# Performance work log

Hardware: AMD Instinct MI355X
Metric: run time of the kernel (lower is better)

Reference implementation:

```python
import jax, jax.numpy as jnp
import numpy as np

# Assumed sub-module definitions (NODETracker repo, sources not provided):
#   MLP(in,out)   = Linear -> LayerNorm -> LeakyReLU(0.1)
#   MLPODEF(dim,hidden,n_layers=2) = Linear(dim->h) -> tanh -> [Linear(h->h) -> tanh]*(n_layers-1) -> Linear(h->dim)
#   ode_solver_factory(None) -> fixed-step RK4, here 4 steps over t in [0,1]

LEAKY = 0.1
N_ODE_STEPS = 4
LATENT_DIM = 512
OBS_DIM = 256
HID_DIM = 1024
STATE = 2 * LATENT_DIM  # 1024
TIME_LEN = 128
BATCH = 512


def mlp_block(x, W, b, g, beta):
    h = x @ W + b
    mu = h.mean(-1, keepdims=True)
    var = ((h - mu) ** 2).mean(-1, keepdims=True)
    h = (h - mu) * jax.lax.rsqrt(var + 1e-5) * g + beta
    return jnp.where(h >= 0, h, LEAKY * h)


def odef(z, p):
    W0, b0, W1, b1, W2, b2 = p
    h = jnp.tanh(z @ W0 + b0)
    h = jnp.tanh(h @ W1 + b1)
    return h @ W2 + b2


def rk4_solve(z, p):
    dt = 1.0 / N_ODE_STEPS
    def step(z, _):
        k1 = odef(z, p)
        k2 = odef(z + 0.5 * dt * k1, p)
        k3 = odef(z + 0.5 * dt * k2, p)
        k4 = odef(z + dt * k3, p)
        return z + (dt / 6.0) * (k1 + 2 * k2 + 2 * k3 + k4), None
    z, _ = jax.lax.scan(step, z, None, length=N_ODE_STEPS)
    return z


def gru_step(x, h, W_ih, W_hh, b_ih, b_hh):
    gi = x @ W_ih.T + b_ih
    gh = h @ W_hh.T + b_hh
    i_r, i_z, i_n = jnp.split(gi, 3, axis=-1)
    h_r, h_z, h_n = jnp.split(gh, 3, axis=-1)
    r = jax.nn.sigmoid(i_r + h_r)
    zg = jax.nn.sigmoid(i_z + h_z)
    n = jnp.tanh(i_n + r * h_n)
    return (1.0 - zg) * n + zg * h


def setup_inputs() -> dict:
    key = jax.random.key(0)
    ks = jax.random.split(key, 16)
    def lin(k, fi, fo):
        return jax.random.normal(k, (fi, fo), jnp.float32) / np.sqrt(fi)
    return {
        'xs': jax.random.normal(ks[0], (TIME_LEN, BATCH, OBS_DIM), jnp.float32),
        'obs_W': lin(ks[1], OBS_DIM, HID_DIM), 'obs_b': jnp.zeros((HID_DIM,), jnp.float32),
        'obs_g': jnp.ones((HID_DIM,), jnp.float32), 'obs_beta': jnp.zeros((HID_DIM,), jnp.float32),
        'lat_W': lin(ks[2], HID_DIM, STATE), 'lat_b': jnp.zeros((STATE,), jnp.float32),
        'lat_g': jnp.ones((STATE,), jnp.float32), 'lat_beta': jnp.zeros((STATE,), jnp.float32),
        'ode_W0': lin(ks[3], STATE, HID_DIM), 'ode_b0': jnp.zeros((HID_DIM,), jnp.float32),
        'ode_W1': lin(ks[4], HID_DIM, HID_DIM), 'ode_b1': jnp.zeros((HID_DIM,), jnp.float32),
        'ode_W2': lin(ks[5], HID_DIM, STATE), 'ode_b2': jnp.zeros((STATE,), jnp.float32),
        'gru_Wih': jax.random.normal(ks[6], (3 * STATE, STATE), jnp.float32) / np.sqrt(STATE),
        'gru_Whh': jax.random.normal(ks[7], (3 * STATE, STATE), jnp.float32) / np.sqrt(STATE),
        'gru_bih': jnp.zeros((3 * STATE,), jnp.float32),
        'gru_bhh': jnp.zeros((3 * STATE,), jnp.float32),
    }


def reference(xs, obs_W, obs_b, obs_g, obs_beta, lat_W, lat_b, lat_g, lat_beta,
              ode_W0, ode_b0, ode_W1, ode_b1, ode_W2, ode_b2,
              gru_Wih, gru_Whh, gru_bih, gru_bhh):
    hs = mlp_block(xs, obs_W, obs_b, obs_g, obs_beta)          # [T,B,hid]
    zs = mlp_block(hs, lat_W, lat_b, lat_g, lat_beta)          # [T,B,2*latent]
    ode_p = (ode_W0, ode_b0, ode_W1, ode_b1, ode_W2, ode_b2)
    batch = xs.shape[1]
    h0 = jnp.zeros((batch, STATE), xs.dtype)

    def step(h, z_t):
        z = rk4_solve(z_t, ode_p)                               # NODE solve from t=0 to 1
        h_new = gru_step(z, h, gru_Wih, gru_Whh, gru_bih, gru_bhh)
        return h_new, None

    z0, _ = jax.lax.scan(step, h0, zs)                          # [B,2*latent]
    return z0[:, :LATENT_DIM], z0[:, LATENT_DIM:]
```

## Files before the change

### kernel.cpp

```cpp
#include <hip/hip_runtime.h>
#include <hip/hip_bf16.h>
#include <hip/hip_cooperative_groups.h>

namespace cg = cooperative_groups;

typedef __bf16 bf16_t;
typedef __bf16 bf16x8 __attribute__((ext_vector_type(8)));
typedef float f32x4 __attribute__((ext_vector_type(4)));

#define TLEN 128
#define BATCHN 512
#define OBS 256
#define HID 1024
#define STATEDIM 1024
#define ROWS (TLEN * BATCHN)
#define RKDT 0.25f

enum { EPI_F32 = 0, EPI_GI, EPI_TANH, EPI_Z0, EPI_KG, EPI_K1, EPI_K2, EPI_K3, EPI_K4 };

__device__ __forceinline__ void gload_lds16(const bf16_t* g, bf16_t* l) {
  __builtin_amdgcn_global_load_lds(
      (const __attribute__((address_space(1))) void*)g,
      (__attribute__((address_space(3))) void*)l, 16, 0, 0);
}

__device__ __forceinline__ bf16_t f2bf(float x) { return (bf16_t)x; }

__device__ __forceinline__ float fast_tanh(float x) {
  const float e = __expf(2.f * x);
  return 1.f - 2.f / (e + 1.f);
}
__device__ __forceinline__ float fast_sigmoid(float x) {
  return 1.f / (1.f + __expf(-x));
}

#define MF(a_, b_, c_) __builtin_amdgcn_mfma_f32_16x16x32_bf16(a_, b_, c_, 0, 0, 0)

template<int EPI>
__global__ __launch_bounds__(256)
void gemm_bt(const bf16_t* __restrict__ A, const bf16_t* __restrict__ Wt,
             const float* __restrict__ bias, int M, int N, int K,
             float* __restrict__ outF, bf16_t* __restrict__ outB,
             float* __restrict__ Z, float* __restrict__ ZN,
             bf16_t* __restrict__ S2, const float* __restrict__ Z0,
             float kgc)
{
  __shared__ __align__(16) bf16_t As[2][128 * 32];
  __shared__ __align__(16) bf16_t Bs[2][128 * 32];
  const int tid = threadIdx.x;
  const int lane = tid & 63;
  const int wave = tid >> 6;
  const int nbn = N >> 7;

  int bid = blockIdx.x;
  {
    const int nwg = gridDim.x;
    const int q = nwg >> 3, r = nwg & 7;
    const int xcd = bid & 7, lid = bid >> 3;
    bid = (xcd < r ? xcd * (q + 1) : r * (q + 1) + (xcd - r) * q) + lid;
  }
  const int bm = bid / nbn;
  const int bn = bid % nbn;
  const int m0 = bm << 7, n0 = bn << 7;
  const int wr = wave >> 1, wc = wave & 1;
  const int srow = tid >> 2;
  const int scol = (tid & 3) << 3;

  f32x4 acc[4][4] = {};
  const int nk = K >> 5;
  int cur = 0;

  {
    const bf16_t* ga = A  + (size_t)(m0 + srow) * K + scol;
    const bf16_t* gb = Wt + (size_t)(n0 + srow) * K + scol;
    bf16_t* la = &As[0][tid * 8];
    bf16_t* lb = &Bs[0][tid * 8];
    gload_lds16(ga, la);
    gload_lds16(ga + (size_t)64 * K, la + 2048);
    gload_lds16(gb, lb);
    gload_lds16(gb + (size_t)64 * K, lb + 2048);
  }

  for (int ks = 0; ks < nk; ++ks) {
    __syncthreads();
    if (ks + 1 < nk) {
      const bf16_t* ga = A  + (size_t)(m0 + srow) * K + (ks + 1) * 32 + scol;
      const bf16_t* gb = Wt + (size_t)(n0 + srow) * K + (ks + 1) * 32 + scol;
      bf16_t* la = &As[cur ^ 1][tid * 8];
      bf16_t* lb = &Bs[cur ^ 1][tid * 8];
      gload_lds16(ga, la);
      gload_lds16(ga + (size_t)64 * K, la + 2048);
      gload_lds16(gb, lb);
      gload_lds16(gb + (size_t)64 * K, lb + 2048);
    }
    const int kb = (lane >> 4) << 3;
    const int rr = lane & 15;
    bf16x8 af[4], bfr[4];
#pragma unroll
    for (int i = 0; i < 4; ++i) {
      af[i]  = *(const bf16x8*)&As[cur][(wr * 64 + i * 16 + rr) * 32 + kb];
      bfr[i] = *(const bf16x8*)&Bs[cur][(wc * 64 + i * 16 + rr) * 32 + kb];
    }
#pragma unroll
    for (int i = 0; i < 4; ++i)
#pragma unroll
      for (int j = 0; j < 4; ++j)
        acc[i][j] = MF(af[i], bfr[j], acc[i][j]);
    cur ^= 1;
  }

  const int cb = n0 + wc * 64 + (lane & 15);
  const int rb = m0 + wr * 64 + ((lane >> 4) << 2);
#pragma unroll
  for (int j = 0; j < 4; ++j) {
    const int c = cb + j * 16;
    float bv = 0.f;
    if constexpr (EPI != EPI_F32 && EPI != EPI_KG) bv = bias[c];
#pragma unroll
    for (int i = 0; i < 4; ++i) {
      const int r0 = rb + i * 16;
#pragma unroll
      for (int r = 0; r < 4; ++r) {
        const size_t idx = (size_t)(r0 + r) * N + c;
        const float v = acc[i][j][r];
        if constexpr (EPI == EPI_F32) {
          outF[idx] = v;
        } else if constexpr (EPI == EPI_GI) {
          outF[idx] = v + bv;
        } else if constexpr (EPI == EPI_TANH) {
          outB[idx] = f2bf(fast_tanh(v + bv));
        } else if constexpr (EPI == EPI_Z0) {
          const float t = v + bv;
          outF[idx] = t;
          outB[idx] = f2bf(fast_tanh(t));
        } else if constexpr (EPI == EPI_KG) {
          outB[idx] = f2bf(fast_tanh(Z0[idx] + kgc * v));
        } else if constexpr (EPI == EPI_K1) {
          const float k = v + bv;
          ZN[idx] = Z[idx] + (RKDT / 6.f) * k;
          outB[idx] = f2bf(k);
        } else if constexpr (EPI == EPI_K2 || EPI == EPI_K3) {
          const float k = v + bv;
          ZN[idx] += (RKDT / 3.f) * k;
          outB[idx] = f2bf(k);
        } else {
          const float k = v + bv;
          const float s = ZN[idx] + (RKDT / 6.f) * k;
          Z[idx] = s;
          const size_t si = (size_t)(r0 + r) * 2048 + c;
          const bf16_t hi = f2bf(s);
          S2[si] = hi;
          S2[si + 1024] = f2bf(s - (float)hi);
        }
      }
    }
  }
}

__global__ __launch_bounds__(512)
void gru_persistent(const float* __restrict__ gi,
                    const bf16_t* __restrict__ Whh,
                    const float* __restrict__ bhh,
                    float* __restrict__ Hf,
                    bf16_t* __restrict__ hb,
                    float* __restrict__ outp,
                    int TS, int t0)
{
  __shared__ __align__(16) bf16_t Bs[48 * 1032];
  const int tid  = threadIdx.x;
  const int lane = tid & 63;
  const int w    = tid >> 6;
  const int rg   = blockIdx.x >> 6;
  const int jg   = blockIdx.x & 63;
  const int r0   = rg << 7;
  const int j0   = jg << 4;

  for (int it = tid; it < 48 * 128; it += 512) {
    const int rr = it >> 7;
    const int co = (it & 127) << 3;
    const int g = rr >> 4, c = rr & 15;
    *(bf16x8*)&Bs[rr * 1032 + co] =
        *(const bf16x8*)&Whh[(size_t)(g * 1024 + j0 + c) * 1024 + co];
  }

  const int myj = j0 + (lane & 15);
  const float bh_r = bhh[myj], bh_z = bhh[1024 + myj], bh_n = bhh[2048 + myj];
  const int rbase = r0 + w * 16 + ((lane >> 4) << 2);

  float h[4];
#pragma unroll
  for (int q = 0; q < 4; ++q) h[q] = Hf[(size_t)(rbase + q) * 1024 + myj];

  __syncthreads();
  cg::grid_group grid = cg::this_grid();

  const int arow = r0 + w * 16 + (lane & 15);
  const int akoff = (lane >> 4) << 3;

  for (int t = t0; t < t0 + TS; ++t) {
    const bf16_t* ap = hb + (size_t)(t & 1) * 512 * 2048 +
                       (size_t)arow * 2048 + akoff;
    f32x4 a0 = {}, a1 = {}, a2 = {};
    const bf16_t* bp0 = &Bs[(0  + (lane & 15)) * 1032 + akoff];
    const bf16_t* bp1 = &Bs[(16 + (lane & 15)) * 1032 + akoff];
    const bf16_t* bp2 = &Bs[(32 + (lane & 15)) * 1032 + akoff];
#pragma unroll 8
    for (int kc = 0; kc < 64; ++kc) {
      const bf16x8 af = *(const bf16x8*)(ap + kc * 32);
      const int kl = (kc * 32) & 1023;
      a0 = MF(af, *(const bf16x8*)(bp0 + kl), a0);
      a1 = MF(af, *(const bf16x8*)(bp1 + kl), a1);
      a2 = MF(af, *(const bf16x8*)(bp2 + kl), a2);
    }
    const float* gir = gi + (size_t)(t - t0) * 512 * 3072;
    bf16_t* hbw = hb + (size_t)((t + 1) & 1) * 512 * 2048;
#pragma unroll
    for (int q = 0; q < 4; ++q) {
      const size_t rr = (size_t)(rbase + q);
      const float ir = gir[rr * 3072 + myj];
      const float iz = gir[rr * 3072 + 1024 + myj];
      const float in = gir[rr * 3072 + 2048 + myj];
      const float rg_ = fast_sigmoid(ir + a0[q] + bh_r);
      const float zg  = fast_sigmoid(iz + a1[q] + bh_z);
      const float n   = fast_tanh(in + rg_ * (a2[q] + bh_n));
      h[q] = (1.f - zg) * n + zg * h[q];
      const bf16_t hi = f2bf(h[q]);
      hbw[rr * 2048 + myj] = hi;
      hbw[rr * 2048 + 1024 + myj] = f2bf(h[q] - (float)hi);
    }
    grid.sync();
  }

#pragma unroll
  for (int q = 0; q < 4; ++q) {
    const int r = rbase + q;
    Hf[(size_t)r * 1024 + myj] = h[q];
    if (myj < 512) outp[(size_t)r * 512 + myj] = h[q];
    else           outp[262144 + (size_t)r * 512 + (myj - 512)] = h[q];
  }
}

template<bool SPLIT>
__global__ __launch_bounds__(256)
void ln_leaky(const float* __restrict__ pre, const float* __restrict__ b,
              const float* __restrict__ g, const float* __restrict__ bet,
              bf16_t* __restrict__ outB, float* __restrict__ zf)
{
  const int row = blockIdx.x;
  const int tid = threadIdx.x;
  const float* p = pre + (size_t)row * 1024;
  float v[4];
  float s = 0.f, s2 = 0.f;
#pragma unroll
  for (int i = 0; i < 4; ++i) {
    const int c = tid + i * 256;
    v[i] = p[c] + b[c];
    s += v[i]; s2 += v[i] * v[i];
  }
#pragma unroll
  for (int o = 32; o; o >>= 1) { s += __shfl_down(s, o); s2 += __shfl_down(s2, o); }
  __shared__ float rs[4], rs2[4];
  if ((tid & 63) == 0) { rs[tid >> 6] = s; rs2[tid >> 6] = s2; }
  __syncthreads();
  s = rs[0] + rs[1] + rs[2] + rs[3];
  s2 = rs2[0] + rs2[1] + rs2[2] + rs2[3];
  const float mu = s * (1.f / 1024.f);
  const float var = s2 * (1.f / 1024.f) - mu * mu;
  const float rstd = rsqrtf(var + 1e-5f);
#pragma unroll
  for (int i = 0; i < 4; ++i) {
    const int c = tid + i * 256;
    float h = (v[i] - mu) * rstd * g[c] + bet[c];
    h = h >= 0.f ? h : 0.1f * h;
    if constexpr (SPLIT) {
      const bf16_t hi = f2bf(h);
      outB[(size_t)row * 2048 + c] = hi;
      outB[(size_t)row * 2048 + 1024 + c] = f2bf(h - (float)hi);
      zf[(size_t)row * 1024 + c] = h;
    } else {
      outB[(size_t)row * 1024 + c] = f2bf(h);
    }
  }
}

__global__ __launch_bounds__(256)
void transpose_bf16(const float* __restrict__ in, bf16_t* __restrict__ out, int R, int C)
{
  __shared__ float t[32][33];
  const int c0 = blockIdx.x * 32, r0 = blockIdx.y * 32;
  const int tx = threadIdx.x & 31, ty = threadIdx.x >> 5;
#pragma unroll
  for (int i = 0; i < 32; i += 8)
    t[ty + i][tx] = in[(size_t)(r0 + ty + i) * C + c0 + tx];
  __syncthreads();
#pragma unroll
  for (int i = 0; i < 32; i += 8)
    out[(size_t)(c0 + ty + i) * R + r0 + tx] = f2bf(t[tx][ty + i]);
}

__global__ __launch_bounds__(256)
void f2b_kernel(const float* __restrict__ in, bf16_t* __restrict__ out, int n)
{
  const int i = blockIdx.x * 256 + threadIdx.x;
  if (i < n) out[i] = f2bf(in[i]);
}

__global__ __launch_bounds__(256)
void dup2_kernel(const bf16_t* __restrict__ in, bf16_t* __restrict__ out, int N, int K)
{
  const int idx = blockIdx.x * 256 + threadIdx.x;
  if (idx >= N * 2 * K) return;
  const int n = idx / (2 * K);
  const int kk = idx - n * 2 * K;
  const int k = kk < K ? kk : kk - K;
  out[idx] = in[(size_t)n * K + k];
}

__global__ void sentinel_kernel(float* out, float code) {
  if (threadIdx.x == 0 && blockIdx.x == 0) out[0] = code;
}

extern "C" void kernel_launch(void* const* d_in, const int* in_sizes, int n_in,
                              void* d_out, int out_size, void* d_ws, size_t ws_size,
                              hipStream_t stream)
{
  const float* xs    = (const float*)d_in[0];
  const float* obs_W = (const float*)d_in[1];
  const float* obs_b = (const float*)d_in[2];
  const float* obs_g = (const float*)d_in[3];
  const float* obs_be= (const float*)d_in[4];
  const float* lat_W = (const float*)d_in[5];
  const float* lat_b = (const float*)d_in[6];
  const float* lat_g = (const float*)d_in[7];
  const float* lat_be= (const float*)d_in[8];
  const float* W0    = (const float*)d_in[9];
  const float* b0    = (const float*)d_in[10];
  const float* W1    = (const float*)d_in[11];
  const float* b1    = (const float*)d_in[12];
  const float* W2    = (const float*)d_in[13];
  const float* b2    = (const float*)d_in[14];
  const float* Wih   = (const float*)d_in[15];
  const float* Whh   = (const float*)d_in[16];
  const float* bih   = (const float*)d_in[17];
  const float* bhh   = (const float*)d_in[18];

  char* ws = (char*)d_ws;
  size_t off = 0;
  auto alloc = [&](size_t bytes) { char* p = ws + off; off += bytes; return p; };

  bf16_t* OBSWT = (bf16_t*)alloc((size_t)HID * OBS * 2);
  bf16_t* LATWT = (bf16_t*)alloc((size_t)STATEDIM * HID * 2);
  bf16_t* W0T   = (bf16_t*)alloc((size_t)HID * STATEDIM * 2);
  bf16_t* W0T2  = (bf16_t*)alloc((size_t)HID * 2048 * 2);
  bf16_t* W1T   = (bf16_t*)alloc((size_t)HID * HID * 2);
  bf16_t* W2T   = (bf16_t*)alloc((size_t)STATEDIM * HID * 2);
  bf16_t* WIH2  = (bf16_t*)alloc((size_t)3072 * 2048 * 2);
  bf16_t* WHHB  = (bf16_t*)alloc((size_t)3072 * 1024 * 2);
  float*  Hf    = (float*)alloc((size_t)512 * 1024 * 4);
  bf16_t* HB2   = (bf16_t*)alloc((size_t)2 * 512 * 2048 * 2);
  bf16_t* WIHB  = (bf16_t*)alloc((size_t)3072 * 1024 * 2);
  bf16_t* XSB   = (bf16_t*)alloc((size_t)ROWS * OBS * 2);
  const size_t staticEnd = off;

  int nc = -1;
  const int ncs[8] = {1, 2, 4, 8, 16, 32, 64, 128};
  for (int i = 0; i < 8; ++i) {
    const size_t R = (size_t)ROWS / ncs[i];
    if (staticEnd + R * 22528 <= ws_size) { nc = ncs[i]; break; }
  }
  if (nc < 0) {
    sentinel_kernel<<<1, 1, 0, stream>>>((float*)d_out,
                                         -(1000000.0f + (float)(ws_size >> 20)));
    return;
  }
  const int R = ROWS / nc;
  char* arena = ws + staticEnd;
  float*  A1f  = (float*)(arena);
  float*  A2f  = (float*)(arena + (size_t)R * 4096);
  float*  Z0f  = (float*)(arena + (size_t)R * 8192);
  bf16_t* H1b  = (bf16_t*)(arena + (size_t)R * 12288);
  bf16_t* H2b  = (bf16_t*)(arena + (size_t)R * 14336);
  bf16_t* KB   = (bf16_t*)(arena + (size_t)R * 16384);
  bf16_t* S2b  = (bf16_t*)(arena + (size_t)R * 18432);
  float*  GIf  = (float*)(arena);

  auto gemm = [&](int epi, const bf16_t* A, const bf16_t* Wt, const float* bias,
                  int M, int N, int K, float* oF, bf16_t* oB, float kgc = 0.f) {
    dim3 g((M / 128) * (N / 128)), b(256);
    switch (epi) {
      case EPI_F32:  gemm_bt<EPI_F32><<<g, b, 0, stream>>>(A, Wt, bias, M, N, K, oF, oB, A2f, A1f, S2b, Z0f, kgc); break;
      case EPI_GI:   gemm_bt<EPI_GI><<<g, b, 0, stream>>>(A, Wt, bias, M, N, K, oF, oB, A2f, A1f, S2b, Z0f, kgc); break;
      case EPI_TANH: gemm_bt<EPI_TANH><<<g, b, 0, stream>>>(A, Wt, bias, M, N, K, oF, oB, A2f, A1f, S2b, Z0f, kgc); break;
      case EPI_Z0:   gemm_bt<EPI_Z0><<<g, b, 0, stream>>>(A, Wt, bias, M, N, K, oF, oB, A2f, A1f, S2b, Z0f, kgc); break;
      case EPI_KG:   gemm_bt<EPI_KG><<<g, b, 0, stream>>>(A, Wt, bias, M, N, K, oF, oB, A2f, A1f, S2b, Z0f, kgc); break;
      case EPI_K1:   gemm_bt<EPI_K1><<<g, b, 0, stream>>>(A, Wt, bias, M, N, K, oF, oB, A2f, A1f, S2b, Z0f, kgc); break;
      case EPI_K2:   gemm_bt<EPI_K2><<<g, b, 0, stream>>>(A, Wt, bias, M, N, K, oF, oB, A2f, A1f, S2b, Z0f, kgc); break;
      case EPI_K3:   gemm_bt<EPI_K3><<<g, b, 0, stream>>>(A, Wt, bias, M, N, K, oF, oB, A2f, A1f, S2b, Z0f, kgc); break;
      case EPI_K4:   gemm_bt<EPI_K4><<<g, b, 0, stream>>>(A, Wt, bias, M, N, K, oF, oB, A2f, A1f, S2b, Z0f, kgc); break;
    }
  };

  transpose_bf16<<<dim3(HID / 32, OBS / 32), 256, 0, stream>>>(obs_W, OBSWT, OBS, HID);
  transpose_bf16<<<dim3(STATEDIM / 32, HID / 32), 256, 0, stream>>>(lat_W, LATWT, HID, STATEDIM);
  transpose_bf16<<<dim3(HID / 32, STATEDIM / 32), 256, 0, stream>>>(W0, W0T, STATEDIM, HID);
  dup2_kernel<<<(HID * 2048) / 256, 256, 0, stream>>>(W0T, W0T2, HID, 1024);
  transpose_bf16<<<dim3(HID / 32, HID / 32), 256, 0, stream>>>(W1, W1T, HID, HID);
  transpose_bf16<<<dim3(STATEDIM / 32, HID / 32), 256, 0, stream>>>(W2, W2T, HID, STATEDIM);
  f2b_kernel<<<(3072 * 1024) / 256, 256, 0, stream>>>(Wih, WIHB, 3072 * 1024);
  dup2_kernel<<<(3072 * 2048) / 256, 256, 0, stream>>>(WIHB, WIH2, 3072, 1024);
  f2b_kernel<<<(3072 * 1024) / 256, 256, 0, stream>>>(Whh, WHHB, 3072 * 1024);
  f2b_kernel<<<(ROWS * OBS) / 256, 256, 0, stream>>>(xs, XSB, ROWS * OBS);

  hipMemsetAsync(Hf, 0, (size_t)512 * 1024 * 4, stream);
  hipMemsetAsync(HB2, 0, (size_t)2 * 512 * 2048 * 2, stream);
  const int TS = R / BATCHN;

  for (int c = 0; c < nc; ++c) {
    gemm(EPI_F32, XSB + (size_t)c * R * OBS, OBSWT, nullptr, R, HID, OBS, A1f, nullptr);
    ln_leaky<false><<<R, 256, 0, stream>>>(A1f, obs_b, obs_g, obs_be, H1b, nullptr);
    gemm(EPI_F32, H1b, LATWT, nullptr, R, STATEDIM, HID, A1f, nullptr);
    ln_leaky<true><<<R, 256, 0, stream>>>(A1f, lat_b, lat_g, lat_be, S2b, A2f);

    for (int step = 0; step < 4; ++step) {
      gemm(EPI_Z0, S2b, W0T2, b0, R, HID, 2048, Z0f, H1b);
      gemm(EPI_TANH, H1b, W1T, b1, R, HID, HID, nullptr, H2b);
      gemm(EPI_K1, H2b, W2T, b2, R, STATEDIM, HID, nullptr, KB);
      for (int stg = 1; stg < 4; ++stg) {
        const float cg = (stg < 3) ? 0.5f * RKDT : RKDT;
        gemm(EPI_KG, KB, W0T, nullptr, R, HID, STATEDIM, nullptr, H1b, cg);
        gemm(EPI_TANH, H1b, W1T, b1, R, HID, HID, nullptr, H2b);
        gemm(EPI_K1 + stg, H2b, W2T, b2, R, STATEDIM, HID, nullptr, KB);
      }
    }

    gemm(EPI_GI, S2b, WIH2, bih, R, 3072, 2048, GIf, nullptr);

    {
      const float* giArg = GIf;
      const bf16_t* whhArg = WHHB;
      const float* bhhArg = bhh;
      float* hfArg = Hf;
      bf16_t* hbArg = HB2;
      float* outArg = (float*)d_out;
      int tsArg = TS;
      int t0Arg = c * TS;
      void* args[] = { (void*)&giArg, (void*)&whhArg, (void*)&bhhArg,
                       (void*)&hfArg, (void*)&hbArg, (void*)&outArg,
                       (void*)&tsArg, (void*)&t0Arg };
      hipLaunchCooperativeKernel((const void*)gru_persistent,
                                 dim3(256), dim3(512), args, 0, stream);
    }
  }
}
```

Baseline: 21.63 ms.

## Fold W2·W0 into a combined RK stage weight and use 256-row GEMM tiles

Precomputes W2·W0 (and the matching bias b2·W0) so that each RK stage's k output and the next stage's first-layer preactivation come out of one N=2048 GEMM from H2. This removes the separate KG GEMM and the KB intermediate buffer per stage, replacing a K=1024 GEMM over the KB activations with a wider GEMM that shares its A loads. Each GEMM block now processes two 128-row tiles in sequence and prefetches the second tile's first K-slice, halving the grid. The risk is extra bf16 rounding from the folded W0·W2 product, and fewer concurrent blocks per GEMM.

```diff
diff --git a/kernel.cpp b/kernel.cpp
--- a/kernel.cpp
+++ b/kernel.cpp
@@ -16,7 +16,7 @@
 #define ROWS (TLEN * BATCHN)
 #define RKDT 0.25f
 
-enum { EPI_F32 = 0, EPI_GI, EPI_TANH, EPI_Z0, EPI_KG, EPI_K1, EPI_K2, EPI_K3, EPI_K4 };
+enum { EPI_F32 = 0, EPI_GI, EPI_TANH, EPI_B16, EPI_Z0, EPI_KG1, EPI_KG2, EPI_KG3, EPI_K4 };
 
 __device__ __forceinline__ void gload_lds16(const bf16_t* g, bf16_t* l) {
   __builtin_amdgcn_global_load_lds(
@@ -42,8 +42,7 @@
              const float* __restrict__ bias, int M, int N, int K,
              float* __restrict__ outF, bf16_t* __restrict__ outB,
              float* __restrict__ Z, float* __restrict__ ZN,
-             bf16_t* __restrict__ S2, const float* __restrict__ Z0,
-             float kgc)
+             bf16_t* __restrict__ S2, const float* __restrict__ Z0)
 {
   __shared__ __align__(16) bf16_t As[2][128 * 32];
   __shared__ __align__(16) bf16_t Bs[2][128 * 32];
@@ -59,98 +58,99 @@
     const int xcd = bid & 7, lid = bid >> 3;
     bid = (xcd < r ? xcd * (q + 1) : r * (q + 1) + (xcd - r) * q) + lid;
   }
-  const int bm = bid / nbn;
+  const int bmg = bid / nbn;
   const int bn = bid % nbn;
-  const int m0 = bm << 7, n0 = bn << 7;
+  const int n0 = bn << 7;
   const int wr = wave >> 1, wc = wave & 1;
   const int srow = tid >> 2;
   const int scol = (tid & 3) << 3;
-
-  f32x4 acc[4][4] = {};
   const int nk = K >> 5;
   int cur = 0;
 
-  {
-    const bf16_t* ga = A  + (size_t)(m0 + srow) * K + scol;
-    const bf16_t* gb = Wt + (size_t)(n0 + srow) * K + scol;
-    bf16_t* la = &As[0][tid * 8];
-    bf16_t* lb = &Bs[0][tid * 8];
+  auto stage = [&](int m0s, int kt, int bb) {
+    const bf16_t* ga = A  + (size_t)(m0s + srow) * K + kt * 32 + scol;
+    const bf16_t* gb = Wt + (size_t)(n0 + srow) * K + kt * 32 + scol;
+    bf16_t* la = &As[bb][tid * 8];
+    bf16_t* lb = &Bs[bb][tid * 8];
     gload_lds16(ga, la);
     gload_lds16(ga + (size_t)64 * K, la + 2048);
     gload_lds16(gb, lb);
     gload_lds16(gb + (size_t)64 * K, lb + 2048);
-  }
-
-  for (int ks = 0; ks < nk; ++ks) {
-    __syncthreads();
-    if (ks + 1 < nk) {
-      const bf16_t* ga = A  + (size_t)(m0 + srow) * K + (ks + 1) * 32 + scol;
-      const bf16_t* gb = Wt + (size_t)(n0 + srow) * K + (ks + 1) * 32 + scol;
-      bf16_t* la = &As[cur ^ 1][tid * 8];
-      bf16_t* lb = &Bs[cur ^ 1][tid * 8];
-      gload_lds16(ga, la);
-      gload_lds16(ga + (size_t)64 * K, la + 2048);
-      gload_lds16(gb, lb);
-      gload_lds16(gb + (size_t)64 * K, lb + 2048);
-    }
-    const int kb = (lane >> 4) << 3;
-    const int rr = lane & 15;
-    bf16x8 af[4], bfr[4];
-#pragma unroll
-    for (int i = 0; i < 4; ++i) {
-      af[i]  = *(const bf16x8*)&As[cur][(wr * 64 + i * 16 + rr) * 32 + kb];
-      bfr[i] = *(const bf16x8*)&Bs[cur][(wc * 64 + i * 16 + rr) * 32 + kb];
-    }
-#pragma unroll
-    for (int i = 0; i < 4; ++i)
-#pragma unroll
-      for (int j = 0; j < 4; ++j)
-        acc[i][j] = MF(af[i], bfr[j], acc[i][j]);
-    cur ^= 1;
-  }
-
-  const int cb = n0 + wc * 64 + (lane & 15);
-  const int rb = m0 + wr * 64 + ((lane >> 4) << 2);
-#pragma unroll
-  for (int j = 0; j < 4; ++j) {
-    const int c = cb + j * 16;
-    float bv = 0.f;
-    if constexpr (EPI != EPI_F32 && EPI != EPI_KG) bv = bias[c];
-#pragma unroll
-    for (int i = 0; i < 4; ++i) {
-      const int r0 = rb + i * 16;
-#pragma unroll
-      for (int r = 0; r < 4; ++r) {
-        const size_t idx = (size_t)(r0 + r) * N + c;
-        const float v = acc[i][j][r];
-        if constexpr (EPI == EPI_F32) {
-          outF[idx] = v;
-        } else if constexpr (EPI == EPI_GI) {
-          outF[idx] = v + bv;
-        } else if constexpr (EPI == EPI_TANH) {
-          outB[idx] = f2bf(fast_tanh(v + bv));
-        } else if constexpr (EPI == EPI_Z0) {
-          const float t = v + bv;
-          outF[idx] = t;
-          outB[idx] = f2bf(fast_tanh(t));
-        } else if constexpr (EPI == EPI_KG) {
-          outB[idx] = f2bf(fast_tanh(Z0[idx] + kgc * v));
-        } else if constexpr (EPI == EPI_K1) {
-          const float k = v + bv;
-          ZN[idx] = Z[idx] + (RKDT / 6.f) * k;
-          outB[idx] = f2bf(k);
-        } else if constexpr (EPI == EPI_K2 || EPI == EPI_K3) {
-          const float k = v + bv;
-          ZN[idx] += (RKDT / 3.f) * k;
-          outB[idx] = f2bf(k);
-        } else {
-          const float k = v + bv;
-          const float s = ZN[idx] + (RKDT / 6.f) * k;
-          Z[idx] = s;
-          const size_t si = (size_t)(r0 + r) * 2048 + c;
-          const bf16_t hi = f2bf(s);
-          S2[si] = hi;
-          S2[si + 1024] = f2bf(s - (float)hi);
+  };
+
+  stage(bmg * 256, 0, 0);
+
+  for (int t = 0; t < 2; ++t) {
+    const int m0 = bmg * 256 + t * 128;
+    f32x4 acc[4][4] = {};
+
+    for (int ks = 0; ks < nk; ++ks) {
+      __syncthreads();
+      if (ks + 1 < nk)      stage(m0, ks + 1, cur ^ 1);
+      else if (t == 0)      stage(m0 + 128, 0, cur ^ 1);
+      const int kb = (lane >> 4) << 3;
+      const int rr = lane & 15;
+      bf16x8 af[4], bfr[4];
+#pragma unroll
+      for (int i = 0; i < 4; ++i) {
+        af[i]  = *(const bf16x8*)&As[cur][(wr * 64 + i * 16 + rr) * 32 + kb];
+        bfr[i] = *(const bf16x8*)&Bs[cur][(wc * 64 + i * 16 + rr) * 32 + kb];
+      }
+#pragma unroll
+      for (int i = 0; i < 4; ++i)
+#pragma unroll
+        for (int j = 0; j < 4; ++j)
+          acc[i][j] = MF(af[i], bfr[j], acc[i][j]);
+      cur ^= 1;
+    }
+
+    const int cb = n0 + wc * 64 + (lane & 15);
+    const int rb = m0 + wr * 64 + ((lane >> 4) << 2);
+#pragma unroll
+    for (int j = 0; j < 4; ++j) {
+      const int c = cb + j * 16;
+      float bv = 0.f;
+      if constexpr (EPI != EPI_F32 && EPI != EPI_B16) bv = bias[c];
+#pragma unroll
+      for (int i = 0; i < 4; ++i) {
+        const int r0 = rb + i * 16;
+#pragma unroll
+        for (int r = 0; r < 4; ++r) {
+          const size_t idx = (size_t)(r0 + r) * N + c;
+          const float v = acc[i][j][r];
+          if constexpr (EPI == EPI_F32) {
+            outF[idx] = v;
+          } else if constexpr (EPI == EPI_GI) {
+            outF[idx] = v + bv;
+          } else if constexpr (EPI == EPI_TANH) {
+            outB[idx] = f2bf(fast_tanh(v + bv));
+          } else if constexpr (EPI == EPI_B16) {
+            outB[idx] = f2bf(v);
+          } else if constexpr (EPI == EPI_Z0) {
+            const float tz = v + bv;
+            outF[idx] = tz;
+            outB[idx] = f2bf(fast_tanh(tz));
+          } else if constexpr (EPI == EPI_KG1 || EPI == EPI_KG2 || EPI == EPI_KG3) {
+            if (c < 1024) {
+              const size_t ki = (size_t)(r0 + r) * 1024 + c;
+              const float k = v + bv;
+              if constexpr (EPI == EPI_KG1) ZN[ki] = Z[ki] + (RKDT / 6.f) * k;
+              else                          ZN[ki] += (RKDT / 3.f) * k;
+            } else {
+              const size_t gi_ = (size_t)(r0 + r) * 1024 + (c - 1024);
+              const float G = v + bv;
+              const float cg = (EPI == EPI_KG3) ? RKDT : 0.5f * RKDT;
+              outB[gi_] = f2bf(fast_tanh(Z0[gi_] + cg * G));
+            }
+          } else {
+            const float k = v + bv;
+            const float s = ZN[idx] + (RKDT / 6.f) * k;
+            Z[idx] = s;
+            const size_t si = (size_t)(r0 + r) * 2048 + c;
+            const bf16_t hi = f2bf(s);
+            S2[si] = hi;
+            S2[si + 1024] = f2bf(s - (float)hi);
+          }
         }
       }
     }
@@ -314,6 +314,18 @@
   const int kk = idx - n * 2 * K;
   const int k = kk < K ? kk : kk - K;
   out[idx] = in[(size_t)n * K + k];
+}
+
+__global__ __launch_bounds__(256)
+void biaskg_kernel(const float* __restrict__ b2, const float* __restrict__ W0,
+                   float* __restrict__ biasKG)
+{
+  const int n = blockIdx.x * 256 + threadIdx.x;
+  if (n >= 1024) return;
+  biasKG[n] = b2[n];
+  float s = 0.f;
+  for (int ss = 0; ss < 1024; ++ss) s += b2[ss] * W0[(size_t)ss * 1024 + n];
+  biasKG[1024 + n] = s;
 }
 
 __global__ void sentinel_kernel(float* out, float code) {
@@ -353,20 +365,22 @@
   bf16_t* W0T   = (bf16_t*)alloc((size_t)HID * STATEDIM * 2);
   bf16_t* W0T2  = (bf16_t*)alloc((size_t)HID * 2048 * 2);
   bf16_t* W1T   = (bf16_t*)alloc((size_t)HID * HID * 2);
-  bf16_t* W2T   = (bf16_t*)alloc((size_t)STATEDIM * HID * 2);
+  bf16_t* WKG   = (bf16_t*)alloc((size_t)2048 * 1024 * 2);
+  bf16_t* W2B   = (bf16_t*)alloc((size_t)HID * STATEDIM * 2);
   bf16_t* WIH2  = (bf16_t*)alloc((size_t)3072 * 2048 * 2);
   bf16_t* WHHB  = (bf16_t*)alloc((size_t)3072 * 1024 * 2);
   float*  Hf    = (float*)alloc((size_t)512 * 1024 * 4);
   bf16_t* HB2   = (bf16_t*)alloc((size_t)2 * 512 * 2048 * 2);
   bf16_t* WIHB  = (bf16_t*)alloc((size_t)3072 * 1024 * 2);
   bf16_t* XSB   = (bf16_t*)alloc((size_t)ROWS * OBS * 2);
+  float*  biasKG= (float*)alloc((size_t)2048 * 4);
   const size_t staticEnd = off;
 
   int nc = -1;
   const int ncs[8] = {1, 2, 4, 8, 16, 32, 64, 128};
   for (int i = 0; i < 8; ++i) {
     const size_t R = (size_t)ROWS / ncs[i];
-    if (staticEnd + R * 22528 <= ws_size) { nc = ncs[i]; break; }
+    if (staticEnd + R * 20480 <= ws_size) { nc = ncs[i]; break; }
   }
   if (nc < 0) {
     sentinel_kernel<<<1, 1, 0, stream>>>((float*)d_out,
@@ -380,23 +394,22 @@
   float*  Z0f  = (float*)(arena + (size_t)R * 8192);
   bf16_t* H1b  = (bf16_t*)(arena + (size_t)R * 12288);
   bf16_t* H2b  = (bf16_t*)(arena + (size_t)R * 14336);
-  bf16_t* KB   = (bf16_t*)(arena + (size_t)R * 16384);
-  bf16_t* S2b  = (bf16_t*)(arena + (size_t)R * 18432);
+  bf16_t* S2b  = (bf16_t*)(arena + (size_t)R * 16384);
   float*  GIf  = (float*)(arena);
 
   auto gemm = [&](int epi, const bf16_t* A, const bf16_t* Wt, const float* bias,
-                  int M, int N, int K, float* oF, bf16_t* oB, float kgc = 0.f) {
-    dim3 g((M / 128) * (N / 128)), b(256);
+                  int M, int N, int K, float* oF, bf16_t* oB) {
+    dim3 g((M / 256) * (N / 128)), b(256);
     switch (epi) {
-      case EPI_F32:  gemm_bt<EPI_F32><<<g, b, 0, stream>>>(A, Wt, bias, M, N, K, oF, oB, A2f, A1f, S2b, Z0f, kgc); break;
-      case EPI_GI:   gemm_bt<EPI_GI><<<g, b, 0, stream>>>(A, Wt, bias, M, N, K, oF, oB, A2f, A1f, S2b, Z0f, kgc); break;
-      case EPI_TANH: gemm_bt<EPI_TANH><<<g, b, 0, stream>>>(A, Wt, bias, M, N, K, oF, oB, A2f, A1f, S2b, Z0f, kgc); break;
-      case EPI_Z0:   gemm_bt<EPI_Z0><<<g, b, 0, stream>>>(A, Wt, bias, M, N, K, oF, oB, A2f, A1f, S2b, Z0f, kgc); break;
-      case EPI_KG:   gemm_bt<EPI_KG><<<g, b, 0, stream>>>(A, Wt, bias, M, N, K, oF, oB, A2f, A1f, S2b, Z0f, kgc); break;
-      case EPI_K1:   gemm_bt<EPI_K1><<<g, b, 0, stream>>>(A, Wt, bias, M, N, K, oF, oB, A2f, A1f, S2b, Z0f, kgc); break;
-      case EPI_K2:   gemm_bt<EPI_K2><<<g, b, 0, stream>>>(A, Wt, bias, M, N, K, oF, oB, A2f, A1f, S2b, Z0f, kgc); break;
-      case EPI_K3:   gemm_bt<EPI_K3><<<g, b, 0, stream>>>(A, Wt, bias, M, N, K, oF, oB, A2f, A1f, S2b, Z0f, kgc); break;
-      case EPI_K4:   gemm_bt<EPI_K4><<<g, b, 0, stream>>>(A, Wt, bias, M, N, K, oF, oB, A2f, A1f, S2b, Z0f, kgc); break;
+      case EPI_F32:  gemm_bt<EPI_F32><<<g, b, 0, stream>>>(A, Wt, bias, M, N, K, oF, oB, A2f, A1f, S2b, Z0f); break;
+      case EPI_GI:   gemm_bt<EPI_GI><<<g, b, 0, stream>>>(A, Wt, bias, M, N, K, oF, oB, A2f, A1f, S2b, Z0f); break;
+      case EPI_TANH: gemm_bt<EPI_TANH><<<g, b, 0, stream>>>(A, Wt, bias, M, N, K, oF, oB, A2f, A1f, S2b, Z0f); break;
+      case EPI_B16:  gemm_bt<EPI_B16><<<g, b, 0, stream>>>(A, Wt, bias, M, N, K, oF, oB, A2f, A1f, S2b, Z0f); break;
+      case EPI_Z0:   gemm_bt<EPI_Z0><<<g, b, 0, stream>>>(A, Wt, bias, M, N, K, oF, oB, A2f, A1f, S2b, Z0f); break;
+      case EPI_KG1:  gemm_bt<EPI_KG1><<<g, b, 0, stream>>>(A, Wt, bias, M, N, K, oF, oB, A2f, A1f, S2b, Z0f); break;
+      case EPI_KG2:  gemm_bt<EPI_KG2><<<g, b, 0, stream>>>(A, Wt, bias, M, N, K, oF, oB, A2f, A1f, S2b, Z0f); break;
+      case EPI_KG3:  gemm_bt<EPI_KG3><<<g, b, 0, stream>>>(A, Wt, bias, M, N, K, oF, oB, A2f, A1f, S2b, Z0f); break;
+      case EPI_K4:   gemm_bt<EPI_K4><<<g, b, 0, stream>>>(A, Wt, bias, M, N, K, oF, oB, A2f, A1f, S2b, Z0f); break;
     }
   };
 
@@ -405,7 +418,10 @@
   transpose_bf16<<<dim3(HID / 32, STATEDIM / 32), 256, 0, stream>>>(W0, W0T, STATEDIM, HID);
   dup2_kernel<<<(HID * 2048) / 256, 256, 0, stream>>>(W0T, W0T2, HID, 1024);
   transpose_bf16<<<dim3(HID / 32, HID / 32), 256, 0, stream>>>(W1, W1T, HID, HID);
-  transpose_bf16<<<dim3(STATEDIM / 32, HID / 32), 256, 0, stream>>>(W2, W2T, HID, STATEDIM);
+  transpose_bf16<<<dim3(STATEDIM / 32, HID / 32), 256, 0, stream>>>(W2, WKG, HID, STATEDIM);
+  f2b_kernel<<<(HID * STATEDIM) / 256, 256, 0, stream>>>(W2, W2B, HID * STATEDIM);
+  gemm(EPI_B16, W0T, W2B, nullptr, 1024, 1024, 1024, nullptr, WKG + (size_t)1024 * 1024);
+  biaskg_kernel<<<4, 256, 0, stream>>>(b2, W0, biasKG);
   f2b_kernel<<<(3072 * 1024) / 256, 256, 0, stream>>>(Wih, WIHB, 3072 * 1024);
   dup2_kernel<<<(3072 * 2048) / 256, 256, 0, stream>>>(WIHB, WIH2, 3072, 1024);
   f2b_kernel<<<(3072 * 1024) / 256, 256, 0, stream>>>(Whh, WHHB, 3072 * 1024);
@@ -424,13 +440,13 @@
     for (int step = 0; step < 4; ++step) {
       gemm(EPI_Z0, S2b, W0T2, b0, R, HID, 2048, Z0f, H1b);
       gemm(EPI_TANH, H1b, W1T, b1, R, HID, HID, nullptr, H2b);
-      gemm(EPI_K1, H2b, W2T, b2, R, STATEDIM, HID, nullptr, KB);
-      for (int stg = 1; stg < 4; ++stg) {
-        const float cg = (stg < 3) ? 0.5f * RKDT : RKDT;
-        gemm(EPI_KG, KB, W0T, nullptr, R, HID, STATEDIM, nullptr, H1b, cg);
-        gemm(EPI_TANH, H1b, W1T, b1, R, HID, HID, nullptr, H2b);
-        gemm(EPI_K1 + stg, H2b, W2T, b2, R, STATEDIM, HID, nullptr, KB);
-      }
+      gemm(EPI_KG1, H2b, WKG, biasKG, R, 2048, HID, nullptr, H1b);
+      gemm(EPI_TANH, H1b, W1T, b1, R, HID, HID, nullptr, H2b);
+      gemm(EPI_KG2, H2b, WKG, biasKG, R, 2048, HID, nullptr, H1b);
+      gemm(EPI_TANH, H1b, W1T, b1, R, HID, HID, nullptr, H2b);
+      gemm(EPI_KG3, H2b, WKG, biasKG, R, 2048, HID, nullptr, H1b);
+      gemm(EPI_TANH, H1b, W1T, b1, R, HID, HID, nullptr, H2b);
+      gemm(EPI_K4, H2b, WKG, b2, R, STATEDIM, HID, nullptr, nullptr);
     }
 
     gemm(EPI_GI, S2b, WIH2, bih, R, 3072, 2048, GIf, nullptr);
```

Result: slower. 27.54 ms (+27.3%).

## Replace GRU grid.sync with atomic counter barrier and prefetch gate inputs

Applied to the files above, without the earlier changes.

Swaps the cooperative-groups grid.sync in the persistent GRU kernel for a hand-rolled atomic counter barrier: thread 0 of each block increments the counter and spins with s_sleep until it reaches the expected count. The counter is reset by a small kernel before each launch. The next timestep's input-gate values are prefetched into registers before the barrier so their latency overlaps the wait. Hidden-state stores are packed as 32-bit atomic stores via lane shuffles. The aim is to cut per-step barrier overhead and global load latency on the serial recurrence, at the cost of correctness depending on relaxed store and acquire ordering with no explicit release fence.

```diff
diff --git a/kernel.cpp b/kernel.cpp
--- a/kernel.cpp
+++ b/kernel.cpp
@@ -130,9 +130,9 @@
         } else if constexpr (EPI == EPI_TANH) {
           outB[idx] = f2bf(fast_tanh(v + bv));
         } else if constexpr (EPI == EPI_Z0) {
-          const float t = v + bv;
-          outF[idx] = t;
-          outB[idx] = f2bf(fast_tanh(t));
+          const float tz = v + bv;
+          outF[idx] = tz;
+          outB[idx] = f2bf(fast_tanh(tz));
         } else if constexpr (EPI == EPI_KG) {
           outB[idx] = f2bf(fast_tanh(Z0[idx] + kgc * v));
         } else if constexpr (EPI == EPI_K1) {
@@ -163,6 +163,7 @@
                     const float* __restrict__ bhh,
                     float* __restrict__ Hf,
                     bf16_t* __restrict__ hb,
+                    unsigned int* __restrict__ ctr,
                     float* __restrict__ outp,
                     int TS, int t0)
 {
@@ -191,13 +192,26 @@
 #pragma unroll
   for (int q = 0; q < 4; ++q) h[q] = Hf[(size_t)(rbase + q) * 1024 + myj];
 
+  float gpre[12];
+  auto load_gi = [&](int lt) {
+    const float* gir = gi + (size_t)lt * 512 * 3072;
+#pragma unroll
+    for (int q = 0; q < 4; ++q) {
+      const size_t rr = (size_t)(rbase + q);
+      gpre[q * 3 + 0] = gir[rr * 3072 + myj];
+      gpre[q * 3 + 1] = gir[rr * 3072 + 1024 + myj];
+      gpre[q * 3 + 2] = gir[rr * 3072 + 2048 + myj];
+    }
+  };
+  load_gi(0);
+
   __syncthreads();
-  cg::grid_group grid = cg::this_grid();
 
   const int arow = r0 + w * 16 + (lane & 15);
   const int akoff = (lane >> 4) << 3;
 
-  for (int t = t0; t < t0 + TS; ++t) {
+  for (int s = 0; s < TS; ++s) {
+    const int t = t0 + s;
     const bf16_t* ap = hb + (size_t)(t & 1) * 512 * 2048 +
                        (size_t)arow * 2048 + akoff;
     f32x4 a0 = {}, a1 = {}, a2 = {};
@@ -212,23 +226,38 @@
       a1 = MF(af, *(const bf16x8*)(bp1 + kl), a1);
       a2 = MF(af, *(const bf16x8*)(bp2 + kl), a2);
     }
-    const float* gir = gi + (size_t)(t - t0) * 512 * 3072;
     bf16_t* hbw = hb + (size_t)((t + 1) & 1) * 512 * 2048;
 #pragma unroll
     for (int q = 0; q < 4; ++q) {
       const size_t rr = (size_t)(rbase + q);
-      const float ir = gir[rr * 3072 + myj];
-      const float iz = gir[rr * 3072 + 1024 + myj];
-      const float in = gir[rr * 3072 + 2048 + myj];
-      const float rg_ = fast_sigmoid(ir + a0[q] + bh_r);
-      const float zg  = fast_sigmoid(iz + a1[q] + bh_z);
-      const float n   = fast_tanh(in + rg_ * (a2[q] + bh_n));
+      const float rg_ = fast_sigmoid(gpre[q * 3 + 0] + a0[q] + bh_r);
+      const float zg  = fast_sigmoid(gpre[q * 3 + 1] + a1[q] + bh_z);
+      const float n   = fast_tanh(gpre[q * 3 + 2] + rg_ * (a2[q] + bh_n));
       h[q] = (1.f - zg) * n + zg * h[q];
-      const bf16_t hi = f2bf(h[q]);
-      hbw[rr * 2048 + myj] = hi;
-      hbw[rr * 2048 + 1024 + myj] = f2bf(h[q] - (float)hi);
-    }
-    grid.sync();
+      union { __bf16 b; unsigned short u; } uh, ul;
+      uh.b = f2bf(h[q]);
+      ul.b = f2bf(h[q] - (float)uh.b);
+      const unsigned ph = (unsigned)__shfl_xor((int)uh.u, 1) & 0xFFFFu;
+      const unsigned pl = (unsigned)__shfl_xor((int)ul.u, 1) & 0xFFFFu;
+      if (!(lane & 1)) {
+        const unsigned hiw = (unsigned)uh.u | (ph << 16);
+        const unsigned low = (unsigned)ul.u | (pl << 16);
+        __hip_atomic_store((unsigned*)(hbw + rr * 2048 + myj), hiw,
+                           __ATOMIC_RELAXED, __HIP_MEMORY_SCOPE_AGENT);
+        __hip_atomic_store((unsigned*)(hbw + rr * 2048 + 1024 + myj), low,
+                           __ATOMIC_RELAXED, __HIP_MEMORY_SCOPE_AGENT);
+      }
+    }
+    if (s + 1 < TS) load_gi(s + 1);
+
+    __syncthreads();
+    if (tid == 0) {
+      __hip_atomic_fetch_add(ctr, 1u, __ATOMIC_RELAXED, __HIP_MEMORY_SCOPE_AGENT);
+      const unsigned tgt = 256u * (unsigned)(s + 1);
+      while (__hip_atomic_load(ctr, __ATOMIC_ACQUIRE, __HIP_MEMORY_SCOPE_AGENT) < tgt)
+        __builtin_amdgcn_s_sleep(1);
+    }
+    __syncthreads();
   }
 
 #pragma unroll
@@ -238,6 +267,11 @@
     if (myj < 512) outp[(size_t)r * 512 + myj] = h[q];
     else           outp[262144 + (size_t)r * 512 + (myj - 512)] = h[q];
   }
+}
+
+__global__ void gru_reset(unsigned int* ctr) {
+  if (threadIdx.x == 0)
+    __hip_atomic_store(ctr, 0u, __ATOMIC_RELAXED, __HIP_MEMORY_SCOPE_AGENT);
 }
 
 template<bool SPLIT>
@@ -360,6 +394,7 @@
   bf16_t* HB2   = (bf16_t*)alloc((size_t)2 * 512 * 2048 * 2);
   bf16_t* WIHB  = (bf16_t*)alloc((size_t)3072 * 1024 * 2);
   bf16_t* XSB   = (bf16_t*)alloc((size_t)ROWS * OBS * 2);
+  unsigned int* CTR = (unsigned int*)alloc(128);
   const size_t staticEnd = off;
 
   int nc = -1;
@@ -435,18 +470,20 @@
 
     gemm(EPI_GI, S2b, WIH2, bih, R, 3072, 2048, GIf, nullptr);
 
+    gru_reset<<<1, 64, 0, stream>>>(CTR);
     {
       const float* giArg = GIf;
       const bf16_t* whhArg = WHHB;
       const float* bhhArg = bhh;
       float* hfArg = Hf;
       bf16_t* hbArg = HB2;
+      unsigned int* ctrArg = CTR;
       float* outArg = (float*)d_out;
       int tsArg = TS;
       int t0Arg = c * TS;
       void* args[] = { (void*)&giArg, (void*)&whhArg, (void*)&bhhArg,
-                       (void*)&hfArg, (void*)&hbArg, (void*)&outArg,
-                       (void*)&tsArg, (void*)&t0Arg };
+                       (void*)&hfArg, (void*)&hbArg, (void*)&ctrArg,
+                       (void*)&outArg, (void*)&tsArg, (void*)&t0Arg };
       hipLaunchCooperativeKernel((const void*)gru_persistent,
                                  dim3(256), dim3(512), args, 0, stream);
     }
```

New measurement: 18.91 ms. 12.6% less time.
